# Optimization experiments

Measured on AMD Instinct MI355X. Metric: run time of the kernel, lower is better.

Reference implementation:

```python
import jax, jax.numpy as jnp
import numpy as np

M = 41
RHO = M / 2.0          # rho=-1 -> M/2
OVERLAPS = 40

def _get_index():
    S = [(n1, n2)
         for n1 in range(-(M // 2), M // 2)
         for n2 in range(-(M // 2), M // 2)
         if abs(n1 * n2) <= RHO * (M // 2)]
    return np.asarray(S, dtype=np.int32)  # [K,2], K=1600 for defaults

_PAIRS = _get_index()


def setup_inputs() -> dict:
    key = jax.random.key(0)
    ks = jax.random.split(key, 7)
    B, L, N = 2, 2048, 2
    K = _PAIRS.shape[0]
    return {
        "x_real": jax.random.normal(ks[0], (B, L, N), jnp.float32),
        "x_imag": jax.random.normal(ks[1], (B, L, N), jnp.float32),
        "task_info": jax.random.uniform(ks[2], (B, 4), jnp.float32),
        "fc_wr": jax.random.normal(ks[3], (K,), jnp.float32) * 0.02,
        "fc_wi": jax.random.normal(ks[4], (K,), jnp.float32) * 0.02,
        "fc_br": jax.random.normal(ks[5], (1,), jnp.float32) * 0.02,
        "fc_bi": jax.random.normal(ks[6], (1,), jnp.float32) * 0.02,
    }


def reference(x_real, x_imag, task_info, fc_wr, fc_wi, fc_br, fc_bi):
    B, L, N = x_real.shape
    x0 = x_real + 1j * x_imag                      # [B,L,N] complex64
    # get_power: dBm -> Watts per mode
    P = 1e-3 * jnp.power(10.0, task_info[:, 0] / 10.0) / N   # [B]

    xf = jnp.fft.fft(x0, axis=1)                   # [B,L,N]
    idx = jnp.arange(L)
    n1 = jnp.asarray(_PAIRS[:, 0])
    n2 = jnp.asarray(_PAIRS[:, 1])

    # torch.roll(x, s, dim=1)[i] == x[(i - s) % L]; vectorize over all K pairs
    def gather(s):                                  # s: [K]
        return xf[:, (idx[:, None] - s[None, :]) % L, :]   # [B,L,K,N]

    A = gather(n1) * jnp.conj(gather(n1 + n2))      # [B,L,K,N]
    E = (A + jnp.roll(A, 1, axis=-1)) * gather(n2)  # [B,L,K,N]

    w = fc_wr + 1j * fc_wi                          # [K]
    b = fc_br[0] + 1j * fc_bi[0]
    delta = jnp.einsum('blkn,k->bln', E, w) + b     # ComplexLinear K->1
    delta = jnp.fft.ifft(delta, axis=1)

    out = (x0 + delta * P[:, None, None])[:, OVERLAPS // 2 : L - OVERLAPS // 2, :]
    # return real/imag stacked so the baseline output is real-valued
    return jnp.stack([out.real, out.imag], axis=-1)  # [B, L-OVERLAPS, N, 2]
```

## Files before the change

kernel.cpp:

```cpp
#include <hip/hip_runtime.h>


#define L_FFT 2048
#define NB 2
#define NM 2
#define ND 40
#define CROP 20
#define LOUT 2008
#define NT 512
#define TILE 64
#define NGRP 8
#define GHALO 103
#define ANGC 3.0679615757712823e-03f

__device__ __forceinline__ float2 cmul(float2 a, float2 b) {
    return make_float2(a.x*b.x - a.y*b.y, a.x*b.y + a.y*b.x);
}
__device__ __forceinline__ float2 cmulc(float2 a, float2 b) {
    return make_float2(a.x*b.x + a.y*b.y, a.y*b.x - a.x*b.y);
}

template<int SIGN>
__device__ __forceinline__ void r4_bfly(const float2* src, float2* dst, int tid,
                                        int m, float2 w1, float2 w2, float2 w3) {
    int k2 = tid & (m - 1);
    int jm = tid - k2;
    float2 A = src[tid];
    float2 C = src[tid + 512];
    float2 B = src[tid + 1024];
    float2 D = src[tid + 1536];
    float2 T0 = make_float2(A.x + B.x, A.y + B.y);
    float2 T1 = make_float2(A.x - B.x, A.y - B.y);
    float2 T2 = make_float2(C.x + D.x, C.y + D.y);
    float2 cd = make_float2(C.x - D.x, C.y - D.y);
    float2 T3 = (SIGN < 0) ? make_float2(cd.y, -cd.x)
                           : make_float2(-cd.y, cd.x);
    int base = 4 * jm + k2;
    dst[base]       = make_float2(T0.x + T2.x, T0.y + T2.y);
    dst[base + m]   = cmul(make_float2(T1.x + T3.x, T1.y + T3.y), w1);
    dst[base + 2*m] = cmul(make_float2(T0.x - T2.x, T0.y - T2.y), w2);
    dst[base + 3*m] = cmul(make_float2(T1.x - T3.x, T1.y - T3.y), w3);
}

template<int SIGN>
__device__ void fft2048_r4_dual(float2* x0, float2* t0, float2* x1, float2* t1, int tid) {
    float2 *s0 = x0, *d0 = t0, *s1 = x1, *d1 = t1;
    #pragma unroll
    for (int m = 1; m <= 256; m *= 4) {
        __syncthreads();
        int jm = tid - (tid & (m - 1));
        float ang = (float)(SIGN * jm) * ANGC;
        float sv = __sinf(ang), cv = __cosf(ang);
        float2 w1 = make_float2(cv, sv);
        float2 w2 = cmul(w1, w1);
        float2 w3 = cmul(w2, w1);
        r4_bfly<SIGN>(s0, d0, tid, m, w1, w2, w3);
        r4_bfly<SIGN>(s1, d1, tid, m, w1, w2, w3);
        float2* t;
        t = s0; s0 = d0; d0 = t;
        t = s1; s1 = d1; d1 = t;
    }
    __syncthreads();
    #pragma unroll
    for (int it = 0; it < 2; ++it) {
        int q = tid + it * 512;
        float2 a0 = s0[q], b0 = s0[q + 1024];
        d0[q]        = make_float2(a0.x + b0.x, a0.y + b0.y);
        d0[q + 1024] = make_float2(a0.x - b0.x, a0.y - b0.y);
        float2 a1 = s1[q], b1 = s1[q + 1024];
        d1[q]        = make_float2(a1.x + b1.x, a1.y + b1.y);
        d1[q + 1024] = make_float2(a1.x - b1.x, a1.y - b1.y);
    }
    __syncthreads();
}

template<int SIGN>
__device__ void fft2048_r4(float2* bufA, float2* bufB, const float2* tw, int tid) {
    float2* src = bufA;
    float2* dst = bufB;
    #pragma unroll
    for (int m = 1; m <= 256; m *= 4) {
        __syncthreads();
        int jm = tid - (tid & (m - 1));
        float2 w1 = tw[jm];
        float2 w2 = cmul(w1, w1);
        float2 w3 = cmul(w2, w1);
        r4_bfly<SIGN>(src, dst, tid, m, w1, w2, w3);
        float2* t = src; src = dst; dst = t;
    }
    __syncthreads();
    #pragma unroll
    for (int it = 0; it < 2; ++it) {
        int q = tid + it * 512;
        float2 a = src[q];
        float2 b = src[q + 1024];
        dst[q]        = make_float2(a.x + b.x, a.y + b.y);
        dst[q + 1024] = make_float2(a.x - b.x, a.y - b.y);
    }
    __syncthreads();
}

template<int SIGN>
__device__ void build_tw(float2* tw, int tid) {
    if (tid < 512) {
        float ang = (float)(SIGN * tid) * ANGC;
        tw[tid] = make_float2(__cosf(ang), __sinf(ang));
    }
}

__global__ __launch_bounds__(NT, 2) void gs2_kernel(const float* __restrict__ xr,
                                                    const float* __restrict__ xi,
                                                    const float* __restrict__ wr,
                                                    const float* __restrict__ wi,
                                                    float2* __restrict__ df) {
    __shared__ float2 xs0[L_FFT];
    __shared__ float2 xs1[L_FFT];
    __shared__ float2 scr0[L_FFT];
    __shared__ float2 scr1[L_FFT];

    int blk = blockIdx.x;
    int b   = blk >> 5;
    int l0  = (blk & 31) * TILE;
    int tid = threadIdx.x;

    const float2* xr2 = (const float2*)xr;
    const float2* xi2 = (const float2*)xi;
    for (int t = tid; t < L_FFT; t += NT) {
        float2 re = xr2[b * L_FFT + t];
        float2 im = xi2[b * L_FFT + t];
        xs0[t] = make_float2(re.x, im.x);
        xs1[t] = make_float2(re.y, im.y);
    }

    fft2048_r4_dual<-1>(xs0, scr0, xs1, scr1, tid);

    float2* Gs  = scr0;
    float2* pr0 = scr1;
    float2* pr1 = scr1 + NT;

    int grp = tid >> 6;
    int lt  = tid & 63;
    int l   = l0 + lt;
    float2 acc0 = make_float2(0.f, 0.f);
    float2 acc1 = make_float2(0.f, 0.f);

    #pragma unroll 1
    for (int it = 0; it < 5; ++it) {
        int d  = it * NGRP + grp;
        int dd = d - 20;
        __syncthreads();
        #pragma unroll
        for (int p = 0; p < 2; ++p) {
            int j = lt + p * 64;
            if (j < GHALO) {
                int m = l0 - 19 + j;
                float2 g0 = cmulc(xs0[m & (L_FFT-1)], xs0[(m - dd) & (L_FFT-1)]);
                float2 g1 = cmulc(xs1[m & (L_FFT-1)], xs1[(m - dd) & (L_FFT-1)]);
                Gs[grp * GHALO + j] = make_float2(g0.x + g1.x, g0.y + g1.y);
            }
        }
        __syncthreads();
        float2 s2 = make_float2(0.f, 0.f);
        #pragma unroll 4
        for (int n1i = 0; n1i < ND; ++n1i) {
            float2 g = Gs[grp * GHALO + lt + 39 - n1i];
            float wxr = wr[n1i * ND + d], wxi = wi[n1i * ND + d];
            s2.x += wxr * g.x - wxi * g.y;
            s2.y += wxr * g.y + wxi * g.x;
        }
        float2 xv0 = xs0[(l - dd) & (L_FFT-1)];
        float2 xv1 = xs1[(l - dd) & (L_FFT-1)];
        float2 c0 = cmul(s2, xv0);
        float2 c1 = cmul(s2, xv1);
        acc0.x += c0.x; acc0.y += c0.y;
        acc1.x += c1.x; acc1.y += c1.y;
    }
    __syncthreads();
    pr0[tid] = acc0;
    pr1[tid] = acc1;
    __syncthreads();
    if (tid < 128) {
        int n = tid >> 6, lq = tid & 63;
        float2* pr = n ? pr1 : pr0;
        float2 s = make_float2(0.f, 0.f);
        #pragma unroll
        for (int g = 0; g < NGRP; ++g) {
            float2 v = pr[g * 64 + lq];
            s.x += v.x; s.y += v.y;
        }
        df[(b * 2 + n) * L_FFT + l0 + lq] = s;
    }
}

__global__ __launch_bounds__(NT) void ifft_out_kernel(const float2* __restrict__ df,
                                                      const float* __restrict__ xr,
                                                      const float* __restrict__ xi,
                                                      const float* __restrict__ task,
                                                      float* __restrict__ out) {
    __shared__ float2 bufA[L_FFT];
    __shared__ float2 bufB[L_FFT];
    __shared__ float2 tw[512];
    int bn = blockIdx.x;
    int b = bn >> 1, n = bn & 1;
    int tid = threadIdx.x;
    const float2* dfreq = df + bn * L_FFT;
    #pragma unroll
    for (int it = 0; it < 4; ++it)
        bufA[tid + it * NT] = dfreq[tid + it * NT];
    build_tw<1>(tw, tid);
    fft2048_r4<1>(bufA, bufB, tw, tid);
    float P = 1e-3f * __powf(10.f, task[b * 4] * 0.1f) * 0.5f;
    float scale = P * (1.0f / (float)L_FFT);
    for (int t = CROP + tid; t < L_FFT - CROP; t += NT) {
        int gi = (b * L_FFT + t) * NM + n;
        float2 dv = bufA[t];
        int oi = ((b * LOUT + (t - CROP)) * NM + n) * 2;
        out[oi]     = xr[gi] + dv.x * scale;
        out[oi + 1] = xi[gi] + dv.y * scale;
    }
}

extern "C" void kernel_launch(void* const* d_in, const int* in_sizes, int n_in,
                              void* d_out, int out_size, void* d_ws, size_t ws_size,
                              hipStream_t stream) {
    const float* xr   = (const float*)d_in[0];
    const float* xi   = (const float*)d_in[1];
    const float* task = (const float*)d_in[2];
    const float* wr   = (const float*)d_in[3];
    const float* wi   = (const float*)d_in[4];
    float* out = (float*)d_out;

    float2* df = (float2*)d_ws;

    hipLaunchKernelGGL(gs2_kernel,      dim3(64), dim3(NT), 0, stream, xr, xi, wr, wi, df);
    hipLaunchKernelGGL(ifft_out_kernel, dim3(NB * NM), dim3(NT), 0, stream, df, xr, xi, task, out);
}
```

Measured before the change: 23.91 us.

## Fuse inverse FFT into main kernel via per-tile partial DFT with atomic accumulation

The separate inverse-FFT kernel, which ran only 4 blocks, is removed. Each of the 64 main-kernel blocks now computes a direct partial inverse DFT of its 64 frequency bins onto all 2048 output positions and atomically adds the result into the output. A small init kernel first writes the cropped input x into the output. This spreads the inverse transform across all blocks, but it adds O(L*TILE) complex work per block, many float atomics, sequential twiddle recurrence error, and it still needs two launches.

```diff
diff --git a/kernel.cpp b/kernel.cpp
--- a/kernel.cpp
+++ b/kernel.cpp
@@ -74,45 +74,25 @@
     __syncthreads();
 }
 
-template<int SIGN>
-__device__ void fft2048_r4(float2* bufA, float2* bufB, const float2* tw, int tid) {
-    float2* src = bufA;
-    float2* dst = bufB;
-    #pragma unroll
-    for (int m = 1; m <= 256; m *= 4) {
-        __syncthreads();
-        int jm = tid - (tid & (m - 1));
-        float2 w1 = tw[jm];
-        float2 w2 = cmul(w1, w1);
-        float2 w3 = cmul(w2, w1);
-        r4_bfly<SIGN>(src, dst, tid, m, w1, w2, w3);
-        float2* t = src; src = dst; dst = t;
-    }
-    __syncthreads();
-    #pragma unroll
-    for (int it = 0; it < 2; ++it) {
-        int q = tid + it * 512;
-        float2 a = src[q];
-        float2 b = src[q + 1024];
-        dst[q]        = make_float2(a.x + b.x, a.y + b.y);
-        dst[q + 1024] = make_float2(a.x - b.x, a.y - b.y);
-    }
-    __syncthreads();
-}
-
-template<int SIGN>
-__device__ void build_tw(float2* tw, int tid) {
-    if (tid < 512) {
-        float ang = (float)(SIGN * tid) * ANGC;
-        tw[tid] = make_float2(__cosf(ang), __sinf(ang));
-    }
+__global__ __launch_bounds__(NT) void out_init_kernel(const float* __restrict__ xr,
+                                                      const float* __restrict__ xi,
+                                                      float* __restrict__ out) {
+    int p = blockIdx.x * NT + threadIdx.x;
+    if (p >= NB * LOUT * NM) return;
+    int n  = p & 1;
+    int to = (p >> 1) % LOUT;
+    int b  = p / (LOUT * NM);
+    int gi = (b * L_FFT + to + CROP) * NM + n;
+    out[p * 2]     = xr[gi];
+    out[p * 2 + 1] = xi[gi];
 }
 
 __global__ __launch_bounds__(NT, 2) void gs2_kernel(const float* __restrict__ xr,
                                                     const float* __restrict__ xi,
                                                     const float* __restrict__ wr,
                                                     const float* __restrict__ wi,
-                                                    float2* __restrict__ df) {
+                                                    const float* __restrict__ task,
+                                                    float* __restrict__ out) {
     __shared__ float2 xs0[L_FFT];
     __shared__ float2 xs1[L_FFT];
     __shared__ float2 scr0[L_FFT];
@@ -134,9 +114,10 @@
 
     fft2048_r4_dual<-1>(xs0, scr0, xs1, scr1, tid);
 
-    float2* Gs  = scr0;
-    float2* pr0 = scr1;
-    float2* pr1 = scr1 + NT;
+    float2* Gs    = scr0;
+    float2* pr0   = scr1;
+    float2* pr1   = scr1 + NT;
+    float2* dtile = scr0;
 
     int grp = tid >> 6;
     int lt  = tid & 63;
@@ -188,35 +169,38 @@
             float2 v = pr[g * 64 + lq];
             s.x += v.x; s.y += v.y;
         }
-        df[(b * 2 + n) * L_FFT + l0 + lq] = s;
-    }
-}
-
-__global__ __launch_bounds__(NT) void ifft_out_kernel(const float2* __restrict__ df,
-                                                      const float* __restrict__ xr,
-                                                      const float* __restrict__ xi,
-                                                      const float* __restrict__ task,
-                                                      float* __restrict__ out) {
-    __shared__ float2 bufA[L_FFT];
-    __shared__ float2 bufB[L_FFT];
-    __shared__ float2 tw[512];
-    int bn = blockIdx.x;
-    int b = bn >> 1, n = bn & 1;
-    int tid = threadIdx.x;
-    const float2* dfreq = df + bn * L_FFT;
-    #pragma unroll
-    for (int it = 0; it < 4; ++it)
-        bufA[tid + it * NT] = dfreq[tid + it * NT];
-    build_tw<1>(tw, tid);
-    fft2048_r4<1>(bufA, bufB, tw, tid);
-    float P = 1e-3f * __powf(10.f, task[b * 4] * 0.1f) * 0.5f;
-    float scale = P * (1.0f / (float)L_FFT);
-    for (int t = CROP + tid; t < L_FFT - CROP; t += NT) {
-        int gi = (b * L_FFT + t) * NM + n;
-        float2 dv = bufA[t];
-        int oi = ((b * LOUT + (t - CROP)) * NM + n) * 2;
-        out[oi]     = xr[gi] + dv.x * scale;
-        out[oi + 1] = xi[gi] + dv.y * scale;
+        float P = 1e-3f * __powf(10.f, task[b * 4] * 0.1f) * 0.5f;
+        float scale = P * (1.0f / (float)L_FFT);
+        dtile[n * TILE + lq] = make_float2(s.x * scale, s.y * scale);
+    }
+    __syncthreads();
+
+    #pragma unroll 1
+    for (int it = 0; it < 4; ++it) {
+        int t = tid + it * NT;
+        if (t < CROP || t >= L_FFT - CROP) continue;
+        float angr = (float)t * ANGC;
+        float2 r = make_float2(__cosf(angr), __sinf(angr));
+        int a0i = (int)(((long long)l0 * t) & (L_FFT - 1));
+        float ang0 = (float)a0i * ANGC;
+        float2 w = make_float2(__cosf(ang0), __sinf(ang0));
+        float2 s0 = make_float2(0.f, 0.f);
+        float2 s1 = make_float2(0.f, 0.f);
+        #pragma unroll 4
+        for (int j = 0; j < TILE; ++j) {
+            float2 d0 = dtile[j];
+            float2 d1 = dtile[TILE + j];
+            s0.x += d0.x * w.x - d0.y * w.y;
+            s0.y += d0.x * w.y + d0.y * w.x;
+            s1.x += d1.x * w.x - d1.y * w.y;
+            s1.y += d1.x * w.y + d1.y * w.x;
+            w = cmul(w, r);
+        }
+        int oi = (b * LOUT + (t - CROP)) * NM * 2;
+        unsafeAtomicAdd(&out[oi],     s0.x);
+        unsafeAtomicAdd(&out[oi + 1], s0.y);
+        unsafeAtomicAdd(&out[oi + 2], s1.x);
+        unsafeAtomicAdd(&out[oi + 3], s1.y);
     }
 }
 
@@ -230,8 +214,8 @@
     const float* wi   = (const float*)d_in[4];
     float* out = (float*)d_out;
 
-    float2* df = (float2*)d_ws;
-
-    hipLaunchKernelGGL(gs2_kernel,      dim3(64), dim3(NT), 0, stream, xr, xi, wr, wi, df);
-    hipLaunchKernelGGL(ifft_out_kernel, dim3(NB * NM), dim3(NT), 0, stream, df, xr, xi, task, out);
-}
+    hipLaunchKernelGGL(out_init_kernel, dim3((NB * LOUT * NM + NT - 1) / NT), dim3(NT),
+                       0, stream, xr, xi, out);
+    hipLaunchKernelGGL(gs2_kernel, dim3(64), dim3(NT), 0, stream,
+                       xr, xi, wr, wi, task, out);
+}
```

Measured after the change: 45.13 us. 88.8% more time.
